# Kernel optimization log

Measured on AMD Instinct MI355X. Metric: run time of the kernel, lower is better.

Reference implementation:

```python
import jax, jax.numpy as jnp
import numpy as np

H = 40  # hidden size


def _gru_layer(x, wih, whh, bih, bhh):
    """PyTorch-convention GRU layer. x: [B,T,D], wih: [3H,D], whh: [3H,H]."""
    # Precompute input contributions for all timesteps at once.
    xp = jnp.einsum('btd,gd->btg', x, wih) + bih  # [B,T,3H]

    def step(h, xt):
        gh = h @ whh.T + bhh                      # [B,3H]
        xr, xz, xn = jnp.split(xt, 3, axis=-1)
        hr, hz, hn = jnp.split(gh, 3, axis=-1)
        r = jax.nn.sigmoid(xr + hr)
        z = jax.nn.sigmoid(xz + hz)
        n = jnp.tanh(xn + r * hn)
        h = (1.0 - z) * n + z * h
        return h, h

    h0 = jnp.zeros((x.shape[0], H), dtype=x.dtype)
    _, ys = jax.lax.scan(step, h0, xp.transpose(1, 0, 2))  # ys: [T,B,H]
    return ys.transpose(1, 0, 2)


def _mlp(h, w1, b1, w2, b2):
    a = jax.nn.leaky_relu(h @ w1.T + b1, negative_slope=0.01)
    return a @ w2.T + b2


def setup_inputs() -> dict:
    key = jax.random.key(0)
    ks = jax.random.split(key, 16)
    s = 1.0 / np.sqrt(H)
    u = lambda k, shape: jax.random.uniform(k, shape, jnp.float32, -s, s)
    x = jax.random.normal(ks[0], (2048, 512, 20), dtype=jnp.float32)
    inp = {
        'x': x,
        # lay1 layer-0 GRU (input dim 20)
        'g0_wih': u(ks[1], (3 * H, 20)),
        'g0_whh': u(ks[2], (3 * H, H)),
        'g0_bih': u(ks[3], (3 * H,)),
        'g0_bhh': u(ks[4], (3 * H,)),
        # 4 stacked GRUs with 40-dim input: lay1 layer-1, lay3, lay5, lay7
        'g_wih': u(ks[5], (4, 3 * H, H)),
        'g_whh': u(ks[6], (4, 3 * H, H)),
        'g_bih': u(ks[7], (4, 3 * H)),
        'g_bhh': u(ks[8], (4, 3 * H)),
        # MLP first linears (lay2, lay4, lay6, lay8 first Linear)
        'mlp_w1': u(ks[9], (4, H, H)),
        'mlp_b1': u(ks[10], (4, H)),
        # MLP second linears for lay2, lay4, lay6 (40->40)
        'mlp_w2': u(ks[11], (3, H, H)),
        'mlp_b2': u(ks[12], (3, H)),
        # lay8 final Linear(40,1)
        'w_last': u(ks[13], (1, H)),
        'b_last': u(ks[14], (1,)),
    }
    return inp


def reference(x, g0_wih, g0_whh, g0_bih, g0_bhh, g_wih, g_whh, g_bih, g_bhh,
              mlp_w1, mlp_b1, mlp_w2, mlp_b2, w_last, b_last):
    # lay1: 2-layer GRU
    h = _gru_layer(x, g0_wih, g0_whh, g0_bih, g0_bhh)
    h = _gru_layer(h, g_wih[0], g_whh[0], g_bih[0], g_bhh[0])
    # lay2..lay7: MLP then GRU, three times
    for i in range(3):
        h = _mlp(h, mlp_w1[i], mlp_b1[i], mlp_w2[i], mlp_b2[i])
        h = _gru_layer(h, g_wih[i + 1], g_whh[i + 1], g_bih[i + 1], g_bhh[i + 1])
    # lay8: Linear(40,40) + LeakyReLU + Linear(40,1)
    a = jax.nn.leaky_relu(h @ mlp_w1[3].T + mlp_b1[3], negative_slope=0.01)
    t = a @ w_last.T + b_last                     # [B,T,1]
    return jax.nn.sigmoid(t[:, -1])               # [B,1]
```

## Files before the change

kernel.cpp:

```cpp
#include <hip/hip_runtime.h>
#include <hip/hip_fp16.h>
#include <cstdint>
#include <cstddef>

#define T_STEPS 512
#define ROWSP   516
#define HID 40
#define GATES 120

typedef _Float16 half8 __attribute__((ext_vector_type(8)));
typedef _Float16 fp16x2 __attribute__((ext_vector_type(2)));
typedef float f32x4 __attribute__((ext_vector_type(4)));

__device__ __forceinline__ void wavesync() { asm volatile("s_waitcnt lgkmcnt(0)" ::: "memory"); }
__device__ __forceinline__ float bperm(int srclane, float v) {
    return __int_as_float(__builtin_amdgcn_ds_bpermute(srclane << 2, __float_as_int(v)));
}
__device__ __forceinline__ float sigm(float x) { return 1.f / (1.f + __expf(-x)); }

template<int J>
__device__ __forceinline__ fp16x2 ext2(half8 v) {
    return __builtin_shufflevector(v, v, 2 * J, 2 * J + 1);
}

__device__ __forceinline__ float vdot2(fp16x2 a, fp16x2 b, float c) {
    float d;
    asm("v_dot2_f32_f16 %0, %1, %2, %3" : "=v"(d) : "v"(a), "v"(b), "v"(c));
    return d;
}

#if __has_builtin(__builtin_amdgcn_fdot2)
__device__ __forceinline__ float fdot2(fp16x2 a, fp16x2 b, float c) {
    return __builtin_amdgcn_fdot2(a, b, c, false);
}
#else
__device__ __forceinline__ float fdot2(fp16x2 a, fp16x2 b, float c) {
    return c + (float)a[0] * (float)b[0] + (float)a[1] * (float)b[1];
}
#endif

__device__ __forceinline__ size_t rowoff(int row) {
    return ((size_t)(row >> 9) * ROWSP + (row & 511)) * GATES;
}

__global__ __launch_bounds__(256) void prep_pad(
    const float* __restrict__ w, const float* __restrict__ b,
    __half* __restrict__ out, int N, int K, int KPAD)
{
    const int idx = blockIdx.x * 256 + threadIdx.x;
    const int n = idx / KPAD, k = idx - n * KPAD;
    float v = 0.f;
    if (n < N) {
        if (k < K) v = w[n * K + k];
        else if (k == KPAD - 1) v = b[n];
    }
    out[idx] = __float2half(v);
}

__global__ __launch_bounds__(256) void prep_eff(
    const float* __restrict__ g_wih, const float* __restrict__ g_bih,
    const float* __restrict__ w2, const float* __restrict__ b2,
    __half* __restrict__ out)
{
    const int li  = blockIdx.y;
    const int idx = blockIdx.x * 256 + threadIdx.x;
    const int n = idx >> 6, k = idx & 63;
    float v = 0.f;
    if (n < GATES) {
        const float* wrow = g_wih + ((size_t)(li + 1) * GATES + n) * HID;
        if (k < HID) {
            for (int j = 0; j < HID; ++j) v += wrow[j] * w2[((size_t)li * HID + j) * HID + k];
        } else if (k == 63) {
            v = g_bih[(size_t)(li + 1) * GATES + n];
            for (int j = 0; j < HID; ++j) v += wrow[j] * b2[(size_t)li * HID + j];
        }
    }
    out[(size_t)li * 128 * 64 + idx] = __float2half(v);
}

__global__ __launch_bounds__(256) void prep_f16cvt(
    const float* __restrict__ w, _Float16* __restrict__ o, int n)
{
    const int i = blockIdx.x * 256 + threadIdx.x;
    if (i < n) o[i] = (_Float16)w[i];
}

template<int MODE>
__global__ __launch_bounds__(256) void precomp_mfma(
    const void* in_, _Float16* xp,
    const _Float16* __restrict__ wihpad,
    const _Float16* __restrict__ w1pad,
    int nrows)
{
    __shared__ _Float16 s_v[4][1024];
    const int tid  = threadIdx.x;
    const int wid  = tid >> 6, lane = tid & 63;
    const int g    = lane >> 4, r = lane & 15;

    constexpr int KP  = (MODE == 0) ? 32 : 64;
    constexpr int NKS = KP / 32;

    half8 bw[8][NKS];
    #pragma unroll
    for (int t = 0; t < 8; ++t)
        #pragma unroll
        for (int ks = 0; ks < NKS; ++ks)
            bw[t][ks] = *reinterpret_cast<const half8*>(wihpad + (t * 16 + r) * KP + ks * 32 + g * 8);

    half8 b1f[3][2];
    char* myv = nullptr;
    if constexpr (MODE == 2) {
        #pragma unroll
        for (int t = 0; t < 3; ++t)
            #pragma unroll
            for (int ks = 0; ks < 2; ++ks)
                b1f[t][ks] = *reinterpret_cast<const half8*>(w1pad + (t * 16 + r) * 64 + ks * 32 + g * 8);
        myv = (char*)&s_v[wid][0];
        uint4 z; z.x = z.y = z.z = z.w = 0u;
        *reinterpret_cast<uint4*>(myv + lane * 32)      = z;
        *reinterpret_cast<uint4*>(myv + lane * 32 + 16) = z;
        wavesync();
        if (lane < 16)
            *reinterpret_cast<_Float16*>(myv + lane * 128 + (126 ^ ((lane & 7) << 4))) = (_Float16)1.f;
        wavesync();
    }

    const int w0     = blockIdx.x * 4 + wid;
    const int stride = gridDim.x * 64;

    for (int rb = w0 * 16; rb < nrows; rb += stride) {
        half8 a0, a1;
        if constexpr (MODE == 0) {
            const float* xr = (const float*)in_ + (size_t)(rb + r) * 20;
            if (g < 2) {
                const float4 v0 = *reinterpret_cast<const float4*>(xr + g * 8);
                const float4 v1 = *reinterpret_cast<const float4*>(xr + g * 8 + 4);
                a0[0]=(_Float16)v0.x; a0[1]=(_Float16)v0.y; a0[2]=(_Float16)v0.z; a0[3]=(_Float16)v0.w;
                a0[4]=(_Float16)v1.x; a0[5]=(_Float16)v1.y; a0[6]=(_Float16)v1.z; a0[7]=(_Float16)v1.w;
            } else if (g == 2) {
                const float4 v0 = *reinterpret_cast<const float4*>(xr + 16);
                a0[0]=(_Float16)v0.x; a0[1]=(_Float16)v0.y; a0[2]=(_Float16)v0.z; a0[3]=(_Float16)v0.w;
                a0[4]=(_Float16)0.f; a0[5]=(_Float16)0.f; a0[6]=(_Float16)0.f; a0[7]=(_Float16)0.f;
            } else {
                #pragma unroll
                for (int j = 0; j < 8; ++j) a0[j] = (_Float16)0.f;
                a0[7] = (_Float16)1.f;
            }
        } else {
            const _Float16* hr = (const _Float16*)in_ + rowoff(rb + r);
            a0 = *reinterpret_cast<const half8*>(hr + g * 8);
            if (g == 0) {
                a1 = *reinterpret_cast<const half8*>(hr + 32);
            } else {
                #pragma unroll
                for (int j = 0; j < 8; ++j) a1[j] = (_Float16)0.f;
                if (g == 3) a1[7] = (_Float16)1.f;
            }
        }

        if constexpr (MODE == 2) {
            #pragma unroll
            for (int t = 0; t < 3; ++t) {
                f32x4 acc = {0.f, 0.f, 0.f, 0.f};
                acc = __builtin_amdgcn_mfma_f32_16x16x32_f16(a0, b1f[t][0], acc, 0, 0, 0);
                acc = __builtin_amdgcn_mfma_f32_16x16x32_f16(a1, b1f[t][1], acc, 0, 0, 0);
                const int n2 = (t * 16 + r) * 2;
                #pragma unroll
                for (int reg = 0; reg < 4; ++reg) {
                    const int m = g * 4 + reg;
                    float v = acc[reg];
                    v = v > 0.f ? v : 0.01f * v;
                    *reinterpret_cast<_Float16*>(myv + m * 128 + (n2 ^ ((m & 7) << 4))) = (_Float16)v;
                }
            }
            wavesync();
            const int sw = (r & 7) << 4;
            a0 = *reinterpret_cast<const half8*>(myv + r * 128 + ((g * 16) ^ sw));
            a1 = *reinterpret_cast<const half8*>(myv + r * 128 + ((64 + g * 16) ^ sw));
        }

        #pragma unroll
        for (int t = 0; t < 8; ++t) {
            f32x4 acc = {0.f, 0.f, 0.f, 0.f};
            acc = __builtin_amdgcn_mfma_f32_16x16x32_f16(a0, bw[t][0], acc, 0, 0, 0);
            if constexpr (NKS == 2)
                acc = __builtin_amdgcn_mfma_f32_16x16x32_f16(a1, bw[t][1], acc, 0, 0, 0);
            const int n = t * 16 + r;
            if (n < GATES) {
                #pragma unroll
                for (int reg = 0; reg < 4; ++reg) {
                    const int m = g * 4 + reg;
                    xp[rowoff(rb + m) + n] = (_Float16)acc[reg];
                }
            }
        }
    }
}

__global__ __launch_bounds__(64)
__attribute__((amdgpu_waves_per_eu(2, 2)))
void gru_recR(
    __half* __restrict__ xp,
    const _Float16* __restrict__ whh16,
    const float* __restrict__ bhh)
{
    __shared__ __align__(16) _Float16 s_w[GATES * HID];
    __shared__ __align__(16) _Float16 s_h[64];

    const int lane = threadIdx.x;
    const int e    = blockIdx.x;

    for (int idx = lane; idx < (GATES * HID) / 8; idx += 64)
        reinterpret_cast<uint4*>(s_w)[idx] = reinterpret_cast<const uint4*>(whh16)[idx];

    const int gA = lane;
    const int gB = (lane < 40) ? (80 + lane) : ((lane < 56) ? (24 + lane) : lane);
    const float bhA = bhh[gA], bhB = bhh[gB];

    __half* xpb = xp + (size_t)e * ROWSP * GATES;

    float hreg = 0.f;
    s_h[lane] = (_Float16)0.f;
    wavesync();

    fp16x2 wA[20], wB[20];
    {
        const _Float16* wrA = s_w + gA * HID;
        const _Float16* wrB = s_w + gB * HID;
        #pragma unroll
        for (int k = 0; k < 5; ++k) {
            const half8 wa = *reinterpret_cast<const half8*>(wrA + k * 8);
            const half8 wb = *reinterpret_cast<const half8*>(wrB + k * 8);
            wA[4*k+0] = ext2<0>(wa); wB[4*k+0] = ext2<0>(wb);
            wA[4*k+1] = ext2<1>(wa); wB[4*k+1] = ext2<1>(wb);
            wA[4*k+2] = ext2<2>(wa); wB[4*k+2] = ext2<2>(wb);
            wA[4*k+3] = ext2<3>(wa); wB[4*k+3] = ext2<3>(wb);
        }
    }
    wavesync();

    __half a0 = xpb[gA],             c0 = xpb[gB];
    __half a1 = xpb[GATES + gA],     c1 = xpb[GATES + gB];
    __half a2 = xpb[2 * GATES + gA], c2 = xpb[2 * GATES + gB];
    const __half* pfA = xpb + 3 * GATES + gA;
    const __half* pfB = xpb + 3 * GATES + gB;
    __half*       pst = xpb + lane;

    #pragma unroll 4
    for (int t = 0; t < T_STEPS; ++t) {
        const __half a3 = *pfA;  pfA += GATES;
        const __half c3 = *pfB;  pfB += GATES;

        const half8 p0 = *reinterpret_cast<const half8*>(&s_h[0]);
        const half8 p1 = *reinterpret_cast<const half8*>(&s_h[8]);
        const half8 p2 = *reinterpret_cast<const half8*>(&s_h[16]);
        const half8 p3 = *reinterpret_cast<const half8*>(&s_h[24]);
        const half8 p4 = *reinterpret_cast<const half8*>(&s_h[32]);

        float A0 = 0.f, A1 = 0.f, A2 = 0.f, A3 = 0.f;
        float B0 = 0.f, B1 = 0.f, B2 = 0.f, B3 = 0.f;
        A0 = vdot2(ext2<0>(p0), wA[ 0], A0); B0 = vdot2(ext2<0>(p0), wB[ 0], B0);
        A1 = vdot2(ext2<1>(p0), wA[ 1], A1); B1 = vdot2(ext2<1>(p0), wB[ 1], B1);
        A2 = vdot2(ext2<2>(p0), wA[ 2], A2); B2 = vdot2(ext2<2>(p0), wB[ 2], B2);
        A3 = vdot2(ext2<3>(p0), wA[ 3], A3); B3 = vdot2(ext2<3>(p0), wB[ 3], B3);
        A0 = vdot2(ext2<0>(p1), wA[ 4], A0); B0 = vdot2(ext2<0>(p1), wB[ 4], B0);
        A1 = vdot2(ext2<1>(p1), wA[ 5], A1); B1 = vdot2(ext2<1>(p1), wB[ 5], B1);
        A2 = vdot2(ext2<2>(p1), wA[ 6], A2); B2 = vdot2(ext2<2>(p1), wB[ 6], B2);
        A3 = vdot2(ext2<3>(p1), wA[ 7], A3); B3 = vdot2(ext2<3>(p1), wB[ 7], B3);
        A0 = vdot2(ext2<0>(p2), wA[ 8], A0); B0 = vdot2(ext2<0>(p2), wB[ 8], B0);
        A1 = vdot2(ext2<1>(p2), wA[ 9], A1); B1 = vdot2(ext2<1>(p2), wB[ 9], B1);
        A2 = vdot2(ext2<2>(p2), wA[10], A2); B2 = vdot2(ext2<2>(p2), wB[10], B2);
        A3 = vdot2(ext2<3>(p2), wA[11], A3); B3 = vdot2(ext2<3>(p2), wB[11], B3);
        A0 = vdot2(ext2<0>(p3), wA[12], A0); B0 = vdot2(ext2<0>(p3), wB[12], B0);
        A1 = vdot2(ext2<1>(p3), wA[13], A1); B1 = vdot2(ext2<1>(p3), wB[13], B1);
        A2 = vdot2(ext2<2>(p3), wA[14], A2); B2 = vdot2(ext2<2>(p3), wB[14], B2);
        A3 = vdot2(ext2<3>(p3), wA[15], A3); B3 = vdot2(ext2<3>(p3), wB[15], B3);
        A0 = vdot2(ext2<0>(p4), wA[16], A0); B0 = vdot2(ext2<0>(p4), wB[16], B0);
        A1 = vdot2(ext2<1>(p4), wA[17], A1); B1 = vdot2(ext2<1>(p4), wB[17], B1);
        A2 = vdot2(ext2<2>(p4), wA[18], A2); B2 = vdot2(ext2<2>(p4), wB[18], B2);
        A3 = vdot2(ext2<3>(p4), wA[19], A3); B3 = vdot2(ext2<3>(p4), wB[19], B3);

        const float shA = bhA + ((A0 + A2) + (A1 + A3));
        const float shB = bhB + ((B0 + B2) + (B1 + B3));
        const float xA  = __half2float(a0);
        const float xB  = __half2float(c0);
        const float sumA = xA + shA;
        const float sumB = xB + shB;
        const float zA = bperm(40 + lane, sumA);
        const float zB = bperm(16 + lane, sumB);

        const float rr  = sigm(sumA);
        const float z   = sigm((lane < 24) ? zA : zB);
        const float pre = xB + rr * shB;
        const float ex  = __expf(-2.f * pre);
        const float nn  = (1.f - ex) / (1.f + ex);
        hreg = (1.f - z) * nn + z * hreg;
        s_h[lane] = (_Float16)hreg;
        *pst = __float2half(hreg);
        pst += GATES;

        a0 = a1; c0 = c1; a1 = a2; c1 = c2; a2 = a3; c2 = c3;
        wavesync();
    }
}

__global__ __launch_bounds__(256) void final_head(
    const __half* __restrict__ xpbuf,
    float* __restrict__ outp,
    const float* __restrict__ w1, const float* __restrict__ b1,
    const float* __restrict__ wl, const float* __restrict__ bl, int n)
{
    __shared__ float s_w1[HID][HID + 1];
    __shared__ float s_b1[HID];
    __shared__ float s_wl[HID];
    for (int i = threadIdx.x; i < HID * HID; i += 256) s_w1[i / HID][i % HID] = w1[i];
    if (threadIdx.x < HID) { s_b1[threadIdx.x] = b1[threadIdx.x]; s_wl[threadIdx.x] = wl[threadIdx.x]; }
    __syncthreads();
    const int e = blockIdx.x * 256 + threadIdx.x;
    if (e >= n) return;

    const __half* hbase = xpbuf + ((size_t)e * ROWSP + (T_STEPS - 1)) * GATES;
    alignas(16) __half hx[HID];
    const uint4* hr = reinterpret_cast<const uint4*>(hbase);
    #pragma unroll
    for (int q = 0; q < HID / 8; ++q) reinterpret_cast<uint4*>(hx)[q] = hr[q];
    float h[HID];
    #pragma unroll
    for (int k = 0; k < HID; ++k) h[k] = __half2float(hx[k]);

    float acc = bl[0];
    #pragma unroll
    for (int u = 0; u < HID; ++u) {
        float a = s_b1[u];
        #pragma unroll
        for (int d = 0; d < HID; ++d) a += s_w1[u][d] * h[d];
        a = a > 0.f ? a : 0.01f * a;
        acc += a * s_wl[u];
    }
    outp[e] = 1.f / (1.f + __expf(-acc));
}

extern "C" void kernel_launch(void* const* d_in, const int* in_sizes, int n_in,
                              void* d_out, int out_size, void* d_ws, size_t ws_size,
                              hipStream_t stream)
{
    const float* x      = (const float*)d_in[0];
    const float* g0_wih = (const float*)d_in[1];
    const float* g0_whh = (const float*)d_in[2];
    const float* g0_bih = (const float*)d_in[3];
    const float* g0_bhh = (const float*)d_in[4];
    const float* g_wih  = (const float*)d_in[5];
    const float* g_whh  = (const float*)d_in[6];
    const float* g_bih  = (const float*)d_in[7];
    const float* g_bhh  = (const float*)d_in[8];
    const float* mlp_w1 = (const float*)d_in[9];
    const float* mlp_b1 = (const float*)d_in[10];
    const float* mlp_w2 = (const float*)d_in[11];
    const float* mlp_b2 = (const float*)d_in[12];
    const float* w_last = (const float*)d_in[13];
    const float* b_last = (const float*)d_in[14];

    const int B = in_sizes[0] / (T_STEPS * 20);
    float* out = (float*)d_out;

    __half* wsz    = (__half*)d_ws;
    __half* w1pad  = wsz;
    __half* effpad = wsz + 3 * 3072;
    __half* g0pad  = wsz + 9216 + 3 * 8192;
    __half* g1pad  = g0pad + 4096;
    _Float16* whh16 = (_Float16*)(wsz + 46080);
    _Float16* xpbuf = (_Float16*)(wsz + 70080);
    const size_t ws_rem = ws_size - 70080 * sizeof(__half);

    for (int li = 0; li < 3; ++li)
        prep_pad<<<dim3(12), dim3(256), 0, stream>>>(
            mlp_w1 + li * 1600, mlp_b1 + li * 40, w1pad + li * 3072, 40, 40, 64);
    prep_pad<<<dim3(16), dim3(256), 0, stream>>>(g0_wih, g0_bih, g0pad, 120, 20, 32);
    prep_pad<<<dim3(32), dim3(256), 0, stream>>>(g_wih, g_bih, g1pad, 120, 40, 64);
    prep_eff<<<dim3(32, 3), dim3(256), 0, stream>>>(g_wih, g_bih, mlp_w2, mlp_b2, effpad);
    prep_f16cvt<<<dim3(19), dim3(256), 0, stream>>>(g0_whh, whh16, 4800);
    prep_f16cvt<<<dim3(75), dim3(256), 0, stream>>>(g_whh, whh16 + 4800, 19200);

    const size_t per_e = (size_t)ROWSP * GATES * sizeof(__half);
    int CB = B;
    while ((size_t)CB * per_e > ws_rem && CB > 64) CB >>= 1;

    for (int c = 0; c < B; c += CB) {
        const int  nrows = CB * T_STEPS;
        const dim3 pgrd(nrows / 512), pblk(256);
        const dim3 rgrd(CB), rblk(64);
        const float* xc = x + (size_t)c * T_STEPS * 20;

        precomp_mfma<0><<<pgrd, pblk, 0, stream>>>(
            xc, xpbuf, (const _Float16*)g0pad, nullptr, nrows);
        gru_recR<<<rgrd, rblk, 0, stream>>>((__half*)xpbuf, whh16, g0_bhh);

        precomp_mfma<1><<<pgrd, pblk, 0, stream>>>(
            xpbuf, xpbuf, (const _Float16*)g1pad, nullptr, nrows);
        gru_recR<<<rgrd, rblk, 0, stream>>>((__half*)xpbuf, whh16 + 4800, g_bhh + 0 * 120);

        for (int li = 0; li < 3; ++li) {
            precomp_mfma<2><<<pgrd, pblk, 0, stream>>>(
                xpbuf, xpbuf, (const _Float16*)(effpad + li * 8192),
                (const _Float16*)(w1pad + li * 3072), nrows);
            gru_recR<<<rgrd, rblk, 0, stream>>>(
                (__half*)xpbuf, whh16 + 4800 + (li + 1) * 4800, g_bhh + (li + 1) * 120);
        }

        final_head<<<dim3((CB + 255) / 256), dim3(256), 0, stream>>>(
            (const __half*)xpbuf, out + c,
            mlp_w1 + 3 * 1600, mlp_b1 + 3 * 40, w_last, b_last, CB);
    }
}
```

Baseline: 1.660 ms.

## Split GRU recurrence across two waves with shared-memory gate exchange

Measured after the change: 1.897 ms. +14.3%, slower.

```diff
diff --git a/kernel.cpp b/kernel.cpp
--- a/kernel.cpp
+++ b/kernel.cpp
@@ -13,8 +13,10 @@
 typedef float f32x4 __attribute__((ext_vector_type(4)));
 
 __device__ __forceinline__ void wavesync() { asm volatile("s_waitcnt lgkmcnt(0)" ::: "memory"); }
-__device__ __forceinline__ float bperm(int srclane, float v) {
-    return __int_as_float(__builtin_amdgcn_ds_bpermute(srclane << 2, __float_as_int(v)));
+__device__ __forceinline__ void sbar() {
+    asm volatile("s_waitcnt lgkmcnt(0)" ::: "memory");
+    __builtin_amdgcn_s_barrier();
+    asm volatile("" ::: "memory");
 }
 __device__ __forceinline__ float sigm(float x) { return 1.f / (1.f + __expf(-x)); }
 
@@ -28,16 +30,6 @@
     asm("v_dot2_f32_f16 %0, %1, %2, %3" : "=v"(d) : "v"(a), "v"(b), "v"(c));
     return d;
 }
-
-#if __has_builtin(__builtin_amdgcn_fdot2)
-__device__ __forceinline__ float fdot2(fp16x2 a, fp16x2 b, float c) {
-    return __builtin_amdgcn_fdot2(a, b, c, false);
-}
-#else
-__device__ __forceinline__ float fdot2(fp16x2 a, fp16x2 b, float c) {
-    return c + (float)a[0] * (float)b[0] + (float)a[1] * (float)b[1];
-}
-#endif
 
 __device__ __forceinline__ size_t rowoff(int row) {
     return ((size_t)(row >> 9) * ROWSP + (row & 511)) * GATES;
@@ -197,59 +189,54 @@
     }
 }
 
-__global__ __launch_bounds__(64)
-__attribute__((amdgpu_waves_per_eu(2, 2)))
-void gru_recR(
+__global__ __launch_bounds__(128)
+__attribute__((amdgpu_waves_per_eu(4, 4)))
+void gru2w(
     __half* __restrict__ xp,
     const _Float16* __restrict__ whh16,
     const float* __restrict__ bhh)
 {
     __shared__ __align__(16) _Float16 s_w[GATES * HID];
+    __shared__ float  s_sum[80];
+    __shared__ float2 s_n2[40];
     __shared__ __align__(16) _Float16 s_h[64];
 
-    const int lane = threadIdx.x;
-    const int e    = blockIdx.x;
-
-    for (int idx = lane; idx < (GATES * HID) / 8; idx += 64)
+    const int tid = threadIdx.x;
+    const int e   = blockIdx.x;
+    const int g   = (tid < GATES) ? tid : 0;
+
+    for (int idx = tid; idx < (GATES * HID) / 8; idx += 128)
         reinterpret_cast<uint4*>(s_w)[idx] = reinterpret_cast<const uint4*>(whh16)[idx];
 
-    const int gA = lane;
-    const int gB = (lane < 40) ? (80 + lane) : ((lane < 56) ? (24 + lane) : lane);
-    const float bhA = bhh[gA], bhB = bhh[gB];
-
+    const float bh = bhh[g];
     __half* xpb = xp + (size_t)e * ROWSP * GATES;
 
-    float hreg = 0.f;
-    s_h[lane] = (_Float16)0.f;
-    wavesync();
-
-    fp16x2 wA[20], wB[20];
+    if (tid < 64) s_h[tid] = (_Float16)0.f;
+    sbar();
+
+    fp16x2 w[20];
     {
-        const _Float16* wrA = s_w + gA * HID;
-        const _Float16* wrB = s_w + gB * HID;
+        const _Float16* wr = s_w + g * HID;
         #pragma unroll
         for (int k = 0; k < 5; ++k) {
-            const half8 wa = *reinterpret_cast<const half8*>(wrA + k * 8);
-            const half8 wb = *reinterpret_cast<const half8*>(wrB + k * 8);
-            wA[4*k+0] = ext2<0>(wa); wB[4*k+0] = ext2<0>(wb);
-            wA[4*k+1] = ext2<1>(wa); wB[4*k+1] = ext2<1>(wb);
-            wA[4*k+2] = ext2<2>(wa); wB[4*k+2] = ext2<2>(wb);
-            wA[4*k+3] = ext2<3>(wa); wB[4*k+3] = ext2<3>(wb);
+            const half8 wv = *reinterpret_cast<const half8*>(wr + k * 8);
+            w[4*k+0] = ext2<0>(wv);
+            w[4*k+1] = ext2<1>(wv);
+            w[4*k+2] = ext2<2>(wv);
+            w[4*k+3] = ext2<3>(wv);
         }
     }
     wavesync();
 
-    __half a0 = xpb[gA],             c0 = xpb[gB];
-    __half a1 = xpb[GATES + gA],     c1 = xpb[GATES + gB];
-    __half a2 = xpb[2 * GATES + gA], c2 = xpb[2 * GATES + gB];
-    const __half* pfA = xpb + 3 * GATES + gA;
-    const __half* pfB = xpb + 3 * GATES + gB;
-    __half*       pst = xpb + lane;
-
-    #pragma unroll 4
+    float hprev = 0.f;
+
+    __half a0 = xpb[g], a1 = xpb[GATES + g], a2 = xpb[2 * GATES + g];
+    const __half* pf  = xpb + 3 * GATES + g;
+    __half*       pst = xpb + tid;
+
+    #pragma unroll 2
     for (int t = 0; t < T_STEPS; ++t) {
-        const __half a3 = *pfA;  pfA += GATES;
-        const __half c3 = *pfB;  pfB += GATES;
+        const __half a3 = *pf;  pf += GATES;
 
         const half8 p0 = *reinterpret_cast<const half8*>(&s_h[0]);
         const half8 p1 = *reinterpret_cast<const half8*>(&s_h[8]);
@@ -258,49 +245,49 @@
         const half8 p4 = *reinterpret_cast<const half8*>(&s_h[32]);
 
         float A0 = 0.f, A1 = 0.f, A2 = 0.f, A3 = 0.f;
-        float B0 = 0.f, B1 = 0.f, B2 = 0.f, B3 = 0.f;
-        A0 = vdot2(ext2<0>(p0), wA[ 0], A0); B0 = vdot2(ext2<0>(p0), wB[ 0], B0);
-        A1 = vdot2(ext2<1>(p0), wA[ 1], A1); B1 = vdot2(ext2<1>(p0), wB[ 1], B1);
-        A2 = vdot2(ext2<2>(p0), wA[ 2], A2); B2 = vdot2(ext2<2>(p0), wB[ 2], B2);
-        A3 = vdot2(ext2<3>(p0), wA[ 3], A3); B3 = vdot2(ext2<3>(p0), wB[ 3], B3);
-        A0 = vdot2(ext2<0>(p1), wA[ 4], A0); B0 = vdot2(ext2<0>(p1), wB[ 4], B0);
-        A1 = vdot2(ext2<1>(p1), wA[ 5], A1); B1 = vdot2(ext2<1>(p1), wB[ 5], B1);
-        A2 = vdot2(ext2<2>(p1), wA[ 6], A2); B2 = vdot2(ext2<2>(p1), wB[ 6], B2);
-        A3 = vdot2(ext2<3>(p1), wA[ 7], A3); B3 = vdot2(ext2<3>(p1), wB[ 7], B3);
-        A0 = vdot2(ext2<0>(p2), wA[ 8], A0); B0 = vdot2(ext2<0>(p2), wB[ 8], B0);
-        A1 = vdot2(ext2<1>(p2), wA[ 9], A1); B1 = vdot2(ext2<1>(p2), wB[ 9], B1);
-        A2 = vdot2(ext2<2>(p2), wA[10], A2); B2 = vdot2(ext2<2>(p2), wB[10], B2);
-        A3 = vdot2(ext2<3>(p2), wA[11], A3); B3 = vdot2(ext2<3>(p2), wB[11], B3);
-        A0 = vdot2(ext2<0>(p3), wA[12], A0); B0 = vdot2(ext2<0>(p3), wB[12], B0);
-        A1 = vdot2(ext2<1>(p3), wA[13], A1); B1 = vdot2(ext2<1>(p3), wB[13], B1);
-        A2 = vdot2(ext2<2>(p3), wA[14], A2); B2 = vdot2(ext2<2>(p3), wB[14], B2);
-        A3 = vdot2(ext2<3>(p3), wA[15], A3); B3 = vdot2(ext2<3>(p3), wB[15], B3);
-        A0 = vdot2(ext2<0>(p4), wA[16], A0); B0 = vdot2(ext2<0>(p4), wB[16], B0);
-        A1 = vdot2(ext2<1>(p4), wA[17], A1); B1 = vdot2(ext2<1>(p4), wB[17], B1);
-        A2 = vdot2(ext2<2>(p4), wA[18], A2); B2 = vdot2(ext2<2>(p4), wB[18], B2);
-        A3 = vdot2(ext2<3>(p4), wA[19], A3); B3 = vdot2(ext2<3>(p4), wB[19], B3);
-
-        const float shA = bhA + ((A0 + A2) + (A1 + A3));
-        const float shB = bhB + ((B0 + B2) + (B1 + B3));
-        const float xA  = __half2float(a0);
-        const float xB  = __half2float(c0);
-        const float sumA = xA + shA;
-        const float sumB = xB + shB;
-        const float zA = bperm(40 + lane, sumA);
-        const float zB = bperm(16 + lane, sumB);
-
-        const float rr  = sigm(sumA);
-        const float z   = sigm((lane < 24) ? zA : zB);
-        const float pre = xB + rr * shB;
-        const float ex  = __expf(-2.f * pre);
-        const float nn  = (1.f - ex) / (1.f + ex);
-        hreg = (1.f - z) * nn + z * hreg;
-        s_h[lane] = (_Float16)hreg;
-        *pst = __float2half(hreg);
+        A0 = vdot2(ext2<0>(p0), w[ 0], A0);
+        A1 = vdot2(ext2<1>(p0), w[ 1], A1);
+        A2 = vdot2(ext2<2>(p0), w[ 2], A2);
+        A3 = vdot2(ext2<3>(p0), w[ 3], A3);
+        A0 = vdot2(ext2<0>(p1), w[ 4], A0);
+        A1 = vdot2(ext2<1>(p1), w[ 5], A1);
+        A2 = vdot2(ext2<2>(p1), w[ 6], A2);
+        A3 = vdot2(ext2<3>(p1), w[ 7], A3);
+        A0 = vdot2(ext2<0>(p2), w[ 8], A0);
+        A1 = vdot2(ext2<1>(p2), w[ 9], A1);
+        A2 = vdot2(ext2<2>(p2), w[10], A2);
+        A3 = vdot2(ext2<3>(p2), w[11], A3);
+        A0 = vdot2(ext2<0>(p3), w[12], A0);
+        A1 = vdot2(ext2<1>(p3), w[13], A1);
+        A2 = vdot2(ext2<2>(p3), w[14], A2);
+        A3 = vdot2(ext2<3>(p3), w[15], A3);
+        A0 = vdot2(ext2<0>(p4), w[16], A0);
+        A1 = vdot2(ext2<1>(p4), w[17], A1);
+        A2 = vdot2(ext2<2>(p4), w[18], A2);
+        A3 = vdot2(ext2<3>(p4), w[19], A3);
+
+        const float sh = bh + ((A0 + A2) + (A1 + A3));
+        const float xv = __half2float(a0);
+
+        if (tid < 80)         s_sum[tid] = xv + sh;
+        else if (tid < GATES) s_n2[tid - 80] = make_float2(sh, xv);
+        sbar();
+
+        if (tid < HID) {
+            const float rr  = sigm(s_sum[tid]);
+            const float z   = sigm(s_sum[40 + tid]);
+            const float2 n2 = s_n2[tid];
+            const float pre = n2.y + rr * n2.x;
+            const float ex  = __expf(-2.f * pre);
+            const float nn  = (1.f - ex) / (1.f + ex);
+            hprev = (1.f - z) * nn + z * hprev;
+            s_h[tid] = (_Float16)hprev;
+            *pst = __float2half(hprev);
+        }
         pst += GATES;
-
-        a0 = a1; c0 = c1; a1 = a2; c1 = c2; a2 = a3; c2 = c3;
-        wavesync();
+        sbar();
+
+        a0 = a1; a1 = a2; a2 = a3;
     }
 }
 
@@ -388,22 +375,22 @@
     for (int c = 0; c < B; c += CB) {
         const int  nrows = CB * T_STEPS;
         const dim3 pgrd(nrows / 512), pblk(256);
-        const dim3 rgrd(CB), rblk(64);
+        const dim3 rgrd(CB), rblk(128);
         const float* xc = x + (size_t)c * T_STEPS * 20;
 
         precomp_mfma<0><<<pgrd, pblk, 0, stream>>>(
             xc, xpbuf, (const _Float16*)g0pad, nullptr, nrows);
-        gru_recR<<<rgrd, rblk, 0, stream>>>((__half*)xpbuf, whh16, g0_bhh);
+        gru2w<<<rgrd, rblk, 0, stream>>>((__half*)xpbuf, whh16, g0_bhh);
 
         precomp_mfma<1><<<pgrd, pblk, 0, stream>>>(
             xpbuf, xpbuf, (const _Float16*)g1pad, nullptr, nrows);
-        gru_recR<<<rgrd, rblk, 0, stream>>>((__half*)xpbuf, whh16 + 4800, g_bhh + 0 * 120);
+        gru2w<<<rgrd, rblk, 0, stream>>>((__half*)xpbuf, whh16 + 4800, g_bhh + 0 * 120);
 
         for (int li = 0; li < 3; ++li) {
             precomp_mfma<2><<<pgrd, pblk, 0, stream>>>(
                 xpbuf, xpbuf, (const _Float16*)(effpad + li * 8192),
                 (const _Float16*)(w1pad + li * 3072), nrows);
-            gru_recR<<<rgrd, rblk, 0, stream>>>(
+            gru2w<<<rgrd, rblk, 0, stream>>>(
                 (__half*)xpbuf, whh16 + 4800 + (li + 1) * 4800, g_bhh + (li + 1) * 120);
         }
 
```
